# Optimization experiments

Measured on AMD Instinct MI355X. Metric: run time of the kernel, lower is better.

## Reference

```python
import jax, jax.numpy as jnp
import numpy as np
from jax import lax

KERNEL_SIZE = 3
DILATION = 1
STRIDE = 1


def setup_inputs() -> dict:
    key = jax.random.key(0)
    k1, k2, k3, k4 = jax.random.split(key, 4)
    B, C_in, L = 8, 256, 4096
    C_out = 256
    out_len = L - DILATION * (KERNEL_SIZE - 1)  # 4094, 'valid' conv
    x = jax.random.normal(k1, (B, C_in, L), dtype=jnp.float32)
    offsets = jax.random.normal(k2, (B, 1, out_len, KERNEL_SIZE), dtype=jnp.float32)
    fan_in = C_in * KERNEL_SIZE
    weight = jax.random.normal(k3, (C_out, C_in, KERNEL_SIZE), dtype=jnp.float32) / np.sqrt(fan_in)
    bias = jax.random.normal(k4, (C_out,), dtype=jnp.float32) / np.sqrt(fan_in)
    return {"x": x, "offsets": offsets, "weight": weight, "bias": bias}


def reference(x, offsets, weight, bias):
    # x: [B, C, L]; offsets: [B, 1, out_len, K]; weight: [C_out, C, K]
    B, C, L = x.shape
    out_len = offsets.shape[-2]
    K = weight.shape[-1]
    dtype = x.dtype

    # dilated kernel sample positions: linspace(0, dilation*(K-1), K)
    dil_pos = (jnp.arange(K, dtype=dtype) * DILATION)  # [K]
    t0s = (jnp.arange(out_len, dtype=dtype) * STRIDE)[:, None]  # [out_len, 1]

    # continuous sample locations, constrained to [t0, t0 + max(dil_pos)]
    T = t0s + dil_pos + offsets  # [B, 1, out_len, K]
    T = jnp.clip(T, t0s, t0s + dil_pos[-1])

    # integer neighbors (indices are non-differentiable)
    U0 = lax.stop_gradient(
        jnp.clip(jnp.floor(T), 0, L - 2).astype(jnp.int32)
    )  # [B, 1, out_len, K]
    U1 = U0 + 1

    def gather(idx):
        # idx: [B, 1, out_len, K] -> gather along L, broadcast over channels
        flat = jnp.broadcast_to(idx.reshape(B, 1, out_len * K), (B, C, out_len * K))
        return jnp.take_along_axis(x, flat, axis=2).reshape(B, C, out_len, K)

    x0 = gather(U0)
    x1 = gather(U1)

    # linear-interpolation weights (tent kernel), broadcast [B,1,out_len,K]
    w0 = jnp.maximum(0.0, 1.0 - jnp.abs(U0.astype(dtype) - T))
    w1 = jnp.maximum(0.0, 1.0 - jnp.abs(U1.astype(dtype) - T))

    interp = w0 * x0 + w1 * x1  # [B, C, out_len, K]

    # conv1d(flatten(interp), weight, stride=K) == per-position K-tap contraction
    out = jnp.einsum("bctk,ock->bot", interp, weight) + bias[None, :, None]
    return out  # [B, C_out, out_len]
```

## Files before the change

kernel.cpp:

```cpp
#include <hip/hip_runtime.h>
#include <stdint.h>


constexpr int CIN  = 256;
constexpr int LX   = 4096;
constexpr int KT   = 3;
constexpr int OUTL = 4094;
constexpr int COUT = 256;
constexpr int WPOS = 68;
constexpr int NQ   = 24;
constexpr int EPIW = 68;
constexpr int NIT  = 2176;

typedef __attribute__((ext_vector_type(8))) short bf16x8;
typedef __attribute__((ext_vector_type(4))) float f32x4;
typedef __attribute__((ext_vector_type(16))) float f32x16;

__device__ __forceinline__ short f2bf(float f) {
  union { float f; uint32_t u; } v; v.f = f;
  return (short)((v.u + 0x8000u) >> 16);
}
__device__ __forceinline__ float4 loadx4(const float* p, int l) {
  if (l + 3 < LX) return *(const float4*)(p + l);
  float4 v; v.x = v.y = v.z = v.w = 0.f;
  if (l + 0 < LX) v.x = p[l + 0];
  if (l + 1 < LX) v.y = p[l + 1];
  if (l + 2 < LX) v.z = p[l + 2];
  return v;
}

__global__ __launch_bounds__(256) void pack_weights_kernel(
    const float* __restrict__ w, short* __restrict__ ap) {
  const int gid = blockIdx.x * 256 + threadIdx.x;
  if (gid >= NQ * 2 * 8 * 64) return;
  const int l   = gid & 63;
  const int mf  = (gid >> 6) & 7;
  const int h   = (gid >> 9) & 1;
  const int q   = gid >> 10;
  const int ch  = q / 12;
  const int ks  = q % 12;
  const int tap = ks >> 2;
  const int c0  = ch * 128 + (ks & 3) * 32 + h * 16 + (l >> 5) * 8;
  const int row = mf * 32 + (l & 31);
  bf16x8 v;
  #pragma unroll
  for (int j = 0; j < 8; ++j) {
    v[j] = f2bf(w[((size_t)row * CIN + c0 + j) * KT + tap]);
  }
  *(bf16x8*)(ap + (size_t)gid * 8) = v;
}

__global__ __launch_bounds__(512, 4) void deform_gemm_kernel(
    const float* __restrict__ x, const float* __restrict__ off,
    const short* __restrict__ ap, const float* __restrict__ bias,
    float* __restrict__ out) {

  __shared__ __align__(16) char smem[34816 + 16384 + 1024];
  float* Xs    = (float*)smem;
  short* Bp    = (short*)(smem + 34816);
  float* Epi   = (float*)smem;
  float* biasS = (float*)(smem + 51200);

  const int tid  = threadIdx.x;
  const int lane = tid & 63;
  const int wid  = tid >> 6;
  const int l31  = lane & 31;
  const int lh   = lane >> 5;

  const int b    = blockIdx.x & 7;
  const int rest = blockIdx.x >> 3;
  const int th   = rest & 1;
  const int tt   = rest >> 1;
  const int t0   = tt * 128 + th * 64;

  float w0m[3], w1m[3];
  int   d0m[3];
  {
    const int t = t0 + (tid & 63);
    #pragma unroll
    for (int k = 0; k < KT; ++k) {
      float w0 = 0.f, w1 = 0.f; int d0 = 0;
      if (t < OUTL) {
        const float o = off[((size_t)b * OUTL + t) * KT + k];
        float T = (float)(t + k) + o;
        T = fminf(fmaxf(T, (float)t), (float)(t + 2));
        int U0 = (int)T;
        if (U0 > LX - 2) U0 = LX - 2;
        w1 = T - (float)U0;
        w0 = 1.f - w1;
        d0 = U0 - t0;
      }
      w0m[k] = w0; w1m[k] = w1; d0m[k] = d0;
    }
  }
  if (tid < COUT) biasS[tid] = bias[tid];

  f32x16 acc0 = {0.f,0.f,0.f,0.f,0.f,0.f,0.f,0.f,0.f,0.f,0.f,0.f,0.f,0.f,0.f,0.f};
  f32x16 acc1 = {0.f,0.f,0.f,0.f,0.f,0.f,0.f,0.f,0.f,0.f,0.f,0.f,0.f,0.f,0.f,0.f};

  const float* xb = x + (size_t)b * CIN * LX;

  const short* apw = ap + wid * 512 + lane * 8;
  bf16x8 aC0 = *(const bf16x8*)apw;
  bf16x8 aC1 = *(const bf16x8*)(apw + 4096);

  #pragma unroll 1
  for (int ch = 0; ch < 2; ++ch) {
    if (ch) __syncthreads();
    #pragma unroll
    for (int r = 0; r < 5; ++r) {
      const int idx = r * 512 + tid;
      if (idx < NIT) {
        const int c = idx / 17, g = idx - c * 17;
        const float4 v = loadx4(xb + (size_t)(ch * 128 + c) * LX, t0 + 4 * g);
        *(float4*)&Xs[c * WPOS + 4 * g] = v;
      }
    }
    __syncthreads();

    #pragma unroll
    for (int tap = 0; tap < KT; ++tap) {
      if (tap) __syncthreads();

      {
        const int tq = tid & 63;
        const int cb = (tid >> 6) * 16;
        const float w0 = w0m[tap], w1 = w1m[tap];
        const int   d0 = d0m[tap];
        const int swt = (tq & 7) << 3;
        bf16x8 o1, o2;
        #pragma unroll
        for (int j = 0; j < 8; ++j) {
          const float xa0 = Xs[(cb + j) * WPOS + d0];
          const float xa1 = Xs[(cb + j) * WPOS + d0 + 1];
          o1[j] = f2bf(xa0 * w0 + xa1 * w1);
        }
        *(bf16x8*)&Bp[(tq * 128 + cb) ^ swt] = o1;
        #pragma unroll
        for (int j = 0; j < 8; ++j) {
          const float xb0 = Xs[(cb + 8 + j) * WPOS + d0];
          const float xb1 = Xs[(cb + 8 + j) * WPOS + d0 + 1];
          o2[j] = f2bf(xb0 * w0 + xb1 * w1);
        }
        *(bf16x8*)&Bp[(tq * 128 + cb + 8) ^ swt] = o2;
      }
      __syncthreads();

      #pragma unroll 1
      for (int csub = 0; csub < 4; ++csub) {
        const int q  = ch * 12 + tap * 4 + csub;
        const int qn = q < NQ - 1 ? q + 1 : NQ - 1;
        const bf16x8 aN0 = *(const bf16x8*)(apw + (size_t)qn * 8192);
        const bf16x8 aN1 = *(const bf16x8*)(apw + (size_t)qn * 8192 + 4096);

        const int cbase = csub * 32 + lh * 8;
        const int ta = l31,      swa = (ta & 7) << 3;
        const int tb = 32 + l31, swb = (tb & 7) << 3;
        {
          const bf16x8 b00 = *(const bf16x8*)&Bp[(ta * 128 + cbase) ^ swa];
          const bf16x8 b10 = *(const bf16x8*)&Bp[(tb * 128 + cbase) ^ swb];
          acc0 = __builtin_amdgcn_mfma_f32_32x32x16_bf16(aC0, b00, acc0, 0, 0, 0);
          acc1 = __builtin_amdgcn_mfma_f32_32x32x16_bf16(aC0, b10, acc1, 0, 0, 0);
        }
        {
          const bf16x8 b01 = *(const bf16x8*)&Bp[(ta * 128 + cbase + 16) ^ swa];
          const bf16x8 b11 = *(const bf16x8*)&Bp[(tb * 128 + cbase + 16) ^ swb];
          acc0 = __builtin_amdgcn_mfma_f32_32x32x16_bf16(aC1, b01, acc0, 0, 0, 0);
          acc1 = __builtin_amdgcn_mfma_f32_32x32x16_bf16(aC1, b11, acc1, 0, 0, 0);
        }
        aC0 = aN0; aC1 = aN1;
      }
    }
  }

  const size_t obase = (size_t)b * COUT * OUTL;
  #pragma unroll
  for (int p = 0; p < 4; ++p) {
    __syncthreads();
    if ((wid >> 1) == p) {
      const int lrb = (wid & 1) * 32;
      #pragma unroll
      for (int r = 0; r < 16; ++r) {
        const int rowl = (r & 3) + 8 * (r >> 2) + 4 * lh;
        const int grow = p * 64 + lrb + rowl;
        Epi[(lrb + rowl) * EPIW + l31]      = acc0[r] + biasS[grow];
        Epi[(lrb + rowl) * EPIW + 32 + l31] = acc1[r] + biasS[grow];
      }
    }
    __syncthreads();
    const int rr = tid >> 3;
    const int c8 = (tid & 7) * 8;
    float* op = out + obase + (size_t)(p * 64 + rr) * OUTL + t0 + c8;
    const f32x4 v0 = *(const f32x4*)&Epi[rr * EPIW + c8];
    const f32x4 v1 = *(const f32x4*)&Epi[rr * EPIW + c8 + 4];
    if (t0 + c8 + 7 < OUTL) {
      *(f32x4*)op = v0;
      *(f32x4*)(op + 4) = v1;
    } else {
      #pragma unroll
      for (int e = 0; e < 4; ++e) {
        if (t0 + c8 + e < OUTL)     op[e]     = v0[e];
        if (t0 + c8 + 4 + e < OUTL) op[4 + e] = v1[e];
      }
    }
  }
}

extern "C" void kernel_launch(void* const* d_in, const int* in_sizes, int n_in,
                              void* d_out, int out_size, void* d_ws, size_t ws_size,
                              hipStream_t stream) {
  const float* x    = (const float*)d_in[0];
  const float* off  = (const float*)d_in[1];
  const float* wgt  = (const float*)d_in[2];
  const float* bias = (const float*)d_in[3];
  float* out  = (float*)d_out;
  short* ap   = (short*)d_ws;

  pack_weights_kernel<<<dim3(NQ * 2 * 8 * 64 / 256), dim3(256), 0, stream>>>(wgt, ap);
  deform_gemm_kernel<<<dim3(512), dim3(512), 0, stream>>>(x, off, ap, bias, out);
}
```

Baseline: 40.39 us.

## Stage X as transposed bf16 and double-buffer interpolated B tiles

The staged input tile is now stored as bf16 in a position-major, XOR-swizzled layout, so the interpolation step reads two 8-wide vectors instead of sixteen scalar fp32 LDS loads. The interpolated B operand is double-buffered: the next tap's tile is built while MFMAs consume the current one, and the second channel half's input is staged during the last tap's MFMAs. This is meant to hide LDS build and global load latency behind matrix work and cut barriers. The cost is an extra bf16 rounding of x before interpolation, which slightly changes numerics.

```diff
diff --git a/kernel.cpp b/kernel.cpp
--- a/kernel.cpp
+++ b/kernel.cpp
@@ -7,10 +7,10 @@
 constexpr int KT   = 3;
 constexpr int OUTL = 4094;
 constexpr int COUT = 256;
-constexpr int WPOS = 68;
 constexpr int NQ   = 24;
 constexpr int EPIW = 68;
 constexpr int NIT  = 2176;
+constexpr int BPH  = 8192;
 
 typedef __attribute__((ext_vector_type(8))) short bf16x8;
 typedef __attribute__((ext_vector_type(4))) float f32x4;
@@ -19,6 +19,11 @@
 __device__ __forceinline__ short f2bf(float f) {
   union { float f; uint32_t u; } v; v.f = f;
   return (short)((v.u + 0x8000u) >> 16);
+}
+__device__ __forceinline__ float bf2f(short s) {
+  union { uint32_t u; float f; } v;
+  v.u = ((uint32_t)(uint16_t)s) << 16;
+  return v.f;
 }
 __device__ __forceinline__ float4 loadx4(const float* p, int l) {
   if (l + 3 < LX) return *(const float4*)(p + l);
@@ -55,11 +60,11 @@
     const short* __restrict__ ap, const float* __restrict__ bias,
     float* __restrict__ out) {
 
-  __shared__ __align__(16) char smem[34816 + 16384 + 1024];
-  float* Xs    = (float*)smem;
-  short* Bp    = (short*)(smem + 34816);
+  __shared__ __align__(16) char smem[17408 + 2 * 16384 + 1024];
+  short* Xt    = (short*)smem;
+  short* BpB   = (short*)(smem + 17408);
   float* Epi   = (float*)smem;
-  float* biasS = (float*)(smem + 51200);
+  float* biasS = (float*)(smem + 50176);
 
   const int tid  = threadIdx.x;
   const int lane = tid & 63;
@@ -104,79 +109,140 @@
   bf16x8 aC0 = *(const bf16x8*)apw;
   bf16x8 aC1 = *(const bf16x8*)(apw + 4096);
 
+  auto stage = [&](int ch) {
+    #pragma unroll
+    for (int pr = 0; pr < 2; ++pr) {
+      const int i0 = pr * 1024 + tid;
+      const int i1 = i0 + 512;
+      const int c0i = i0 / 17, g0 = i0 - c0i * 17;
+      const int c1i = i1 / 17, g1 = i1 - c1i * 17;
+      const float4 v0 = loadx4(xb + (size_t)(ch * 128 + c0i) * LX, t0 + 4 * g0);
+      const float4 v1 = loadx4(xb + (size_t)(ch * 128 + c1i) * LX, t0 + 4 * g1);
+      const float f0e[4] = {v0.x, v0.y, v0.z, v0.w};
+      const float f1e[4] = {v1.x, v1.y, v1.z, v1.w};
+      #pragma unroll
+      for (int e = 0; e < 4; ++e) {
+        const int p0 = g0 * 4 + e;
+        Xt[(p0 * 128 + c0i) ^ ((p0 & 7) << 3)] = f2bf(f0e[e]);
+      }
+      #pragma unroll
+      for (int e = 0; e < 4; ++e) {
+        const int p1 = g1 * 4 + e;
+        Xt[(p1 * 128 + c1i) ^ ((p1 & 7) << 3)] = f2bf(f1e[e]);
+      }
+    }
+    {
+      const int i4 = 2048 + tid;
+      if (i4 < NIT) {
+        const int c = i4 / 17, g = i4 - c * 17;
+        const float4 v = loadx4(xb + (size_t)(ch * 128 + c) * LX, t0 + 4 * g);
+        const float fe[4] = {v.x, v.y, v.z, v.w};
+        #pragma unroll
+        for (int e = 0; e < 4; ++e) {
+          const int pos = g * 4 + e;
+          Xt[(pos * 128 + c) ^ ((pos & 7) << 3)] = f2bf(fe[e]);
+        }
+      }
+    }
+  };
+
+  auto build = [&](short* Bq, int tap) {
+    const int tq = tid & 63;
+    const int cb = (tid >> 6) * 16;
+    const float w0 = w0m[tap], w1 = w1m[tap];
+    const int   d0 = d0m[tap];
+    const int sw0 = (d0 & 7) << 3;
+    const int sw1 = ((d0 + 1) & 7) << 3;
+    const int r0i = d0 * 128, r1i = (d0 + 1) * 128;
+    const int swt = (tq & 7) << 3;
+    {
+      const bf16x8 r0a = *(const bf16x8*)&Xt[(r0i + cb) ^ sw0];
+      const bf16x8 r1a = *(const bf16x8*)&Xt[(r1i + cb) ^ sw1];
+      bf16x8 o1;
+      #pragma unroll
+      for (int j = 0; j < 8; ++j)
+        o1[j] = f2bf(bf2f(r0a[j]) * w0 + bf2f(r1a[j]) * w1);
+      *(bf16x8*)&Bq[(tq * 128 + cb) ^ swt] = o1;
+    }
+    {
+      const bf16x8 r0b = *(const bf16x8*)&Xt[(r0i + cb + 8) ^ sw0];
+      const bf16x8 r1b = *(const bf16x8*)&Xt[(r1i + cb + 8) ^ sw1];
+      bf16x8 o2;
+      #pragma unroll
+      for (int j = 0; j < 8; ++j)
+        o2[j] = f2bf(bf2f(r0b[j]) * w0 + bf2f(r1b[j]) * w1);
+      *(bf16x8*)&Bq[(tq * 128 + cb + 8) ^ swt] = o2;
+    }
+  };
+
+  auto ksteps = [&](const short* Bq, int p) {
+    #pragma unroll 1
+    for (int csub = 0; csub < 4; ++csub) {
+      const int q  = p * 4 + csub;
+      const int qn = q < NQ - 1 ? q + 1 : NQ - 1;
+      const bf16x8 aN0 = *(const bf16x8*)(apw + (size_t)qn * 8192);
+      const bf16x8 aN1 = *(const bf16x8*)(apw + (size_t)qn * 8192 + 4096);
+
+      const int cbase = csub * 32 + lh * 8;
+      const int ta = l31,      swa = (ta & 7) << 3;
+      const int tb = 32 + l31, swb = (tb & 7) << 3;
+      {
+        const bf16x8 b00 = *(const bf16x8*)&Bq[(ta * 128 + cbase) ^ swa];
+        const bf16x8 b10 = *(const bf16x8*)&Bq[(tb * 128 + cbase) ^ swb];
+        acc0 = __builtin_amdgcn_mfma_f32_32x32x16_bf16(aC0, b00, acc0, 0, 0, 0);
+        acc1 = __builtin_amdgcn_mfma_f32_32x32x16_bf16(aC0, b10, acc1, 0, 0, 0);
+      }
+      {
+        const bf16x8 b01 = *(const bf16x8*)&Bq[(ta * 128 + cbase + 16) ^ swa];
+        const bf16x8 b11 = *(const bf16x8*)&Bq[(tb * 128 + cbase + 16) ^ swb];
+        acc0 = __builtin_amdgcn_mfma_f32_32x32x16_bf16(aC1, b01, acc0, 0, 0, 0);
+        acc1 = __builtin_amdgcn_mfma_f32_32x32x16_bf16(aC1, b11, acc1, 0, 0, 0);
+      }
+      aC0 = aN0; aC1 = aN1;
+    }
+  };
+
+  stage(0);
+  __syncthreads();
+  build(BpB, 0);
+  __syncthreads();
+
   #pragma unroll 1
   for (int ch = 0; ch < 2; ++ch) {
-    if (ch) __syncthreads();
-    #pragma unroll
-    for (int r = 0; r < 5; ++r) {
-      const int idx = r * 512 + tid;
-      if (idx < NIT) {
-        const int c = idx / 17, g = idx - c * 17;
-        const float4 v = loadx4(xb + (size_t)(ch * 128 + c) * LX, t0 + 4 * g);
-        *(float4*)&Xs[c * WPOS + 4 * g] = v;
-      }
-    }
-    __syncthreads();
-
-    #pragma unroll
-    for (int tap = 0; tap < KT; ++tap) {
-      if (tap) __syncthreads();
-
-      {
-        const int tq = tid & 63;
-        const int cb = (tid >> 6) * 16;
-        const float w0 = w0m[tap], w1 = w1m[tap];
-        const int   d0 = d0m[tap];
-        const int swt = (tq & 7) << 3;
-        bf16x8 o1, o2;
-        #pragma unroll
-        for (int j = 0; j < 8; ++j) {
-          const float xa0 = Xs[(cb + j) * WPOS + d0];
-          const float xa1 = Xs[(cb + j) * WPOS + d0 + 1];
-          o1[j] = f2bf(xa0 * w0 + xa1 * w1);
-        }
-        *(bf16x8*)&Bp[(tq * 128 + cb) ^ swt] = o1;
-        #pragma unroll
-        for (int j = 0; j < 8; ++j) {
-          const float xb0 = Xs[(cb + 8 + j) * WPOS + d0];
-          const float xb1 = Xs[(cb + 8 + j) * WPOS + d0 + 1];
-          o2[j] = f2bf(xb0 * w0 + xb1 * w1);
-        }
-        *(bf16x8*)&Bp[(tq * 128 + cb + 8) ^ swt] = o2;
-      }
+    {
+      const int p = ch * 3;
+      short* cur = BpB + (p & 1) * BPH;
+      short* nxt = BpB + ((p + 1) & 1) * BPH;
+      if (ch == 1) {
+        build(cur, 0);
+        __syncthreads();
+      }
+      build(nxt, 1);
+      ksteps(cur, p);
       __syncthreads();
-
-      #pragma unroll 1
-      for (int csub = 0; csub < 4; ++csub) {
-        const int q  = ch * 12 + tap * 4 + csub;
-        const int qn = q < NQ - 1 ? q + 1 : NQ - 1;
-        const bf16x8 aN0 = *(const bf16x8*)(apw + (size_t)qn * 8192);
-        const bf16x8 aN1 = *(const bf16x8*)(apw + (size_t)qn * 8192 + 4096);
-
-        const int cbase = csub * 32 + lh * 8;
-        const int ta = l31,      swa = (ta & 7) << 3;
-        const int tb = 32 + l31, swb = (tb & 7) << 3;
-        {
-          const bf16x8 b00 = *(const bf16x8*)&Bp[(ta * 128 + cbase) ^ swa];
-          const bf16x8 b10 = *(const bf16x8*)&Bp[(tb * 128 + cbase) ^ swb];
-          acc0 = __builtin_amdgcn_mfma_f32_32x32x16_bf16(aC0, b00, acc0, 0, 0, 0);
-          acc1 = __builtin_amdgcn_mfma_f32_32x32x16_bf16(aC0, b10, acc1, 0, 0, 0);
-        }
-        {
-          const bf16x8 b01 = *(const bf16x8*)&Bp[(ta * 128 + cbase + 16) ^ swa];
-          const bf16x8 b11 = *(const bf16x8*)&Bp[(tb * 128 + cbase + 16) ^ swb];
-          acc0 = __builtin_amdgcn_mfma_f32_32x32x16_bf16(aC1, b01, acc0, 0, 0, 0);
-          acc1 = __builtin_amdgcn_mfma_f32_32x32x16_bf16(aC1, b11, acc1, 0, 0, 0);
-        }
-        aC0 = aN0; aC1 = aN1;
-      }
+    }
+    {
+      const int p = ch * 3 + 1;
+      short* cur = BpB + (p & 1) * BPH;
+      short* nxt = BpB + ((p + 1) & 1) * BPH;
+      if (ch == 0) build(nxt, 2);
+      else         build(nxt, 2);
+      ksteps(cur, p);
+      __syncthreads();
+    }
+    {
+      const int p = ch * 3 + 2;
+      short* cur = BpB + (p & 1) * BPH;
+      if (ch == 0) stage(1);
+      ksteps(cur, p);
+      __syncthreads();
     }
   }
 
   const size_t obase = (size_t)b * COUT * OUTL;
   #pragma unroll
   for (int p = 0; p < 4; ++p) {
-    __syncthreads();
+    if (p) __syncthreads();
     if ((wid >> 1) == p) {
       const int lrb = (wid & 1) * 32;
       #pragma unroll
```

Result: slower. 42.37 us (+4.9%).

## Fuse interpolation into MFMA operand loads with bf16 transposed x tile

Applied to the files above, without the earlier changes.

Stores the x tile in shared memory as swizzled bf16 in position-major layout. Each wave now builds its own interpolated A operand in registers directly before the MFMA, which removes the separate interpolated-B staging buffer and the per-tap barriers. The operand roles are swapped: interpolated activations become the A matrix and weights are read from global as the B matrix, with the epilogue transposed to match. Shared memory use shrinks and the launch bounds change, at the cost of double rounding of x to bf16, repeated interpolation work per wave, and unprefetched global weight loads inside the loop.

```diff
diff --git a/kernel.cpp b/kernel.cpp
--- a/kernel.cpp
+++ b/kernel.cpp
@@ -7,9 +7,8 @@
 constexpr int KT   = 3;
 constexpr int OUTL = 4094;
 constexpr int COUT = 256;
-constexpr int WPOS = 68;
 constexpr int NQ   = 24;
-constexpr int EPIW = 68;
+constexpr int EPIT = 65;
 constexpr int NIT  = 2176;
 
 typedef __attribute__((ext_vector_type(8))) short bf16x8;
@@ -19,6 +18,11 @@
 __device__ __forceinline__ short f2bf(float f) {
   union { float f; uint32_t u; } v; v.f = f;
   return (short)((v.u + 0x8000u) >> 16);
+}
+__device__ __forceinline__ float bf2f(short s) {
+  union { uint32_t u; float f; } v;
+  v.u = ((uint32_t)(uint16_t)s) << 16;
+  return v.f;
 }
 __device__ __forceinline__ float4 loadx4(const float* p, int l) {
   if (l + 3 < LX) return *(const float4*)(p + l);
@@ -50,16 +54,15 @@
   *(bf16x8*)(ap + (size_t)gid * 8) = v;
 }
 
-__global__ __launch_bounds__(512, 4) void deform_gemm_kernel(
+__global__ __launch_bounds__(512, 2) void deform_gemm_kernel(
     const float* __restrict__ x, const float* __restrict__ off,
     const short* __restrict__ ap, const float* __restrict__ bias,
     float* __restrict__ out) {
 
-  __shared__ __align__(16) char smem[34816 + 16384 + 1024];
-  float* Xs    = (float*)smem;
-  short* Bp    = (short*)(smem + 34816);
+  __shared__ __align__(16) char smem[17408 + 1024];
+  short* Xt    = (short*)smem;
   float* Epi   = (float*)smem;
-  float* biasS = (float*)(smem + 51200);
+  float* biasS = (float*)(smem + 17408);
 
   const int tid  = threadIdx.x;
   const int lane = tid & 63;
@@ -67,6 +70,9 @@
   const int l31  = lane & 31;
   const int lh   = lane >> 5;
 
+  const int tfrag = wid & 1;
+  const int og    = wid >> 1;
+
   const int b    = blockIdx.x & 7;
   const int rest = blockIdx.x >> 3;
   const int th   = rest & 1;
@@ -76,7 +82,7 @@
   float w0m[3], w1m[3];
   int   d0m[3];
   {
-    const int t = t0 + (tid & 63);
+    const int t = t0 + tfrag * 32 + l31;
     #pragma unroll
     for (int k = 0; k < KT; ++k) {
       float w0 = 0.f, w1 = 0.f; int d0 = 0;
@@ -100,75 +106,69 @@
 
   const float* xb = x + (size_t)b * CIN * LX;
 
-  const short* apw = ap + wid * 512 + lane * 8;
-  bf16x8 aC0 = *(const bf16x8*)apw;
-  bf16x8 aC1 = *(const bf16x8*)(apw + 4096);
-
   #pragma unroll 1
   for (int ch = 0; ch < 2; ++ch) {
     if (ch) __syncthreads();
     #pragma unroll
     for (int r = 0; r < 5; ++r) {
       const int idx = r * 512 + tid;
-      if (idx < NIT) {
+      if (r < 4 || idx < NIT) {
         const int c = idx / 17, g = idx - c * 17;
         const float4 v = loadx4(xb + (size_t)(ch * 128 + c) * LX, t0 + 4 * g);
-        *(float4*)&Xs[c * WPOS + 4 * g] = v;
+        const float fe[4] = {v.x, v.y, v.z, v.w};
+        #pragma unroll
+        for (int e = 0; e < 4; ++e) {
+          const int pos = g * 4 + e;
+          Xt[(pos * 128 + c) ^ ((pos & 7) << 3)] = f2bf(fe[e]);
+        }
       }
     }
     __syncthreads();
 
     #pragma unroll
     for (int tap = 0; tap < KT; ++tap) {
-      if (tap) __syncthreads();
-
-      {
-        const int tq = tid & 63;
-        const int cb = (tid >> 6) * 16;
-        const float w0 = w0m[tap], w1 = w1m[tap];
-        const int   d0 = d0m[tap];
-        const int swt = (tq & 7) << 3;
-        bf16x8 o1, o2;
-        #pragma unroll
-        for (int j = 0; j < 8; ++j) {
-          const float xa0 = Xs[(cb + j) * WPOS + d0];
-          const float xa1 = Xs[(cb + j) * WPOS + d0 + 1];
-          o1[j] = f2bf(xa0 * w0 + xa1 * w1);
-        }
-        *(bf16x8*)&Bp[(tq * 128 + cb) ^ swt] = o1;
-        #pragma unroll
-        for (int j = 0; j < 8; ++j) {
-          const float xb0 = Xs[(cb + 8 + j) * WPOS + d0];
-          const float xb1 = Xs[(cb + 8 + j) * WPOS + d0 + 1];
-          o2[j] = f2bf(xb0 * w0 + xb1 * w1);
-        }
-        *(bf16x8*)&Bp[(tq * 128 + cb + 8) ^ swt] = o2;
-      }
-      __syncthreads();
+      const float w0 = w0m[tap];
+      const float w1 = w1m[tap];
+      const int   d0 = d0m[tap];
+      const int sw0 = (d0 & 7) << 3;
+      const int sw1 = ((d0 + 1) & 7) << 3;
+      const int r0i = d0 * 128, r1i = (d0 + 1) * 128;
 
       #pragma unroll 1
       for (int csub = 0; csub < 4; ++csub) {
-        const int q  = ch * 12 + tap * 4 + csub;
-        const int qn = q < NQ - 1 ? q + 1 : NQ - 1;
-        const bf16x8 aN0 = *(const bf16x8*)(apw + (size_t)qn * 8192);
-        const bf16x8 aN1 = *(const bf16x8*)(apw + (size_t)qn * 8192 + 4096);
-
-        const int cbase = csub * 32 + lh * 8;
-        const int ta = l31,      swa = (ta & 7) << 3;
-        const int tb = 32 + l31, swb = (tb & 7) << 3;
-        {
-          const bf16x8 b00 = *(const bf16x8*)&Bp[(ta * 128 + cbase) ^ swa];
-          const bf16x8 b10 = *(const bf16x8*)&Bp[(tb * 128 + cbase) ^ swb];
-          acc0 = __builtin_amdgcn_mfma_f32_32x32x16_bf16(aC0, b00, acc0, 0, 0, 0);
-          acc1 = __builtin_amdgcn_mfma_f32_32x32x16_bf16(aC0, b10, acc1, 0, 0, 0);
-        }
-        {
-          const bf16x8 b01 = *(const bf16x8*)&Bp[(ta * 128 + cbase + 16) ^ swa];
-          const bf16x8 b11 = *(const bf16x8*)&Bp[(tb * 128 + cbase + 16) ^ swb];
-          acc0 = __builtin_amdgcn_mfma_f32_32x32x16_bf16(aC1, b01, acc0, 0, 0, 0);
-          acc1 = __builtin_amdgcn_mfma_f32_32x32x16_bf16(aC1, b11, acc1, 0, 0, 0);
-        }
-        aC0 = aN0; aC1 = aN1;
+        const int q = ch * 12 + tap * 4 + csub;
+
+        bf16x8 aA0, aA1;
+        {
+          const int cs = csub * 32 + lh * 8;
+          const bf16x8 r0 = *(const bf16x8*)&Xt[(r0i + cs) ^ sw0];
+          const bf16x8 r1 = *(const bf16x8*)&Xt[(r1i + cs) ^ sw1];
+          #pragma unroll
+          for (int j = 0; j < 8; ++j)
+            aA0[j] = f2bf(bf2f(r0[j]) * w0 + bf2f(r1[j]) * w1);
+        }
+        {
+          const int cs = csub * 32 + 16 + lh * 8;
+          const bf16x8 r0 = *(const bf16x8*)&Xt[(r0i + cs) ^ sw0];
+          const bf16x8 r1 = *(const bf16x8*)&Xt[(r1i + cs) ^ sw1];
+          #pragma unroll
+          for (int j = 0; j < 8; ++j)
+            aA1[j] = f2bf(bf2f(r0[j]) * w0 + bf2f(r1[j]) * w1);
+        }
+
+        const short* wq = ap + (size_t)q * 8192 + lane * 8;
+        {
+          const bf16x8 w00 = *(const bf16x8*)(wq + (og * 2) * 512);
+          const bf16x8 w01 = *(const bf16x8*)(wq + 4096 + (og * 2) * 512);
+          acc0 = __builtin_amdgcn_mfma_f32_32x32x16_bf16(aA0, w00, acc0, 0, 0, 0);
+          acc0 = __builtin_amdgcn_mfma_f32_32x32x16_bf16(aA1, w01, acc0, 0, 0, 0);
+        }
+        {
+          const bf16x8 w10 = *(const bf16x8*)(wq + (og * 2 + 1) * 512);
+          const bf16x8 w11 = *(const bf16x8*)(wq + 4096 + (og * 2 + 1) * 512);
+          acc1 = __builtin_amdgcn_mfma_f32_32x32x16_bf16(aA0, w10, acc1, 0, 0, 0);
+          acc1 = __builtin_amdgcn_mfma_f32_32x32x16_bf16(aA1, w11, acc1, 0, 0, 0);
+        }
       }
     }
   }
@@ -177,22 +177,29 @@
   #pragma unroll
   for (int p = 0; p < 4; ++p) {
     __syncthreads();
-    if ((wid >> 1) == p) {
-      const int lrb = (wid & 1) * 32;
+    if (og == p) {
       #pragma unroll
       for (int r = 0; r < 16; ++r) {
-        const int rowl = (r & 3) + 8 * (r >> 2) + 4 * lh;
-        const int grow = p * 64 + lrb + rowl;
-        Epi[(lrb + rowl) * EPIW + l31]      = acc0[r] + biasS[grow];
-        Epi[(lrb + rowl) * EPIW + 32 + l31] = acc1[r] + biasS[grow];
+        const int trow = (r & 3) + 8 * (r >> 2) + 4 * lh;
+        const int tl   = tfrag * 32 + trow;
+        Epi[tl * EPIT + l31] = acc0[r] + biasS[p * 64 + l31];
+      }
+      #pragma unroll
+      for (int r = 0; r < 16; ++r) {
+        const int trow = (r & 3) + 8 * (r >> 2) + 4 * lh;
+        const int tl   = tfrag * 32 + trow;
+        Epi[tl * EPIT + 32 + l31] = acc1[r] + biasS[p * 64 + 32 + l31];
       }
     }
     __syncthreads();
     const int rr = tid >> 3;
     const int c8 = (tid & 7) * 8;
+    float vals[8];
+    #pragma unroll
+    for (int m = 0; m < 8; ++m) vals[m] = Epi[(c8 + m) * EPIT + rr];
+    const f32x4 v0 = {vals[0], vals[1], vals[2], vals[3]};
+    const f32x4 v1 = {vals[4], vals[5], vals[6], vals[7]};
     float* op = out + obase + (size_t)(p * 64 + rr) * OUTL + t0 + c8;
-    const f32x4 v0 = *(const f32x4*)&Epi[rr * EPIW + c8];
-    const f32x4 v1 = *(const f32x4*)&Epi[rr * EPIW + c8 + 4];
     if (t0 + c8 + 7 < OUTL) {
       *(f32x4*)op = v0;
       *(f32x4*)(op + 4) = v1;
```

After: 52.26 us. 1.29x slower.

## Stage full-channel x tile as transposed bf16 in LDS and vectorize interpolation

Applied to the files above, without the earlier changes.

Loads all 256 input channels of the x tile at once, converts to bf16 and stores it position-major with an XOR swizzle. This lets the interpolation step read 8 channels per vector LDS load instead of scalar strided float reads. It also removes the two-pass channel loop and halves the per-tap barriers. The cost is a larger LDS footprint and a lower occupancy bound (3 blocks instead of 4). Rounding x to bf16 before interpolating adds a second rounding step, which slightly lowers accuracy.

```diff
diff --git a/kernel.cpp b/kernel.cpp
--- a/kernel.cpp
+++ b/kernel.cpp
@@ -7,10 +7,10 @@
 constexpr int KT   = 3;
 constexpr int OUTL = 4094;
 constexpr int COUT = 256;
-constexpr int WPOS = 68;
 constexpr int NQ   = 24;
 constexpr int EPIW = 68;
-constexpr int NIT  = 2176;
+constexpr int CW   = 256;
+constexpr int NST  = 4352;
 
 typedef __attribute__((ext_vector_type(8))) short bf16x8;
 typedef __attribute__((ext_vector_type(4))) float f32x4;
@@ -19,6 +19,11 @@
 __device__ __forceinline__ short f2bf(float f) {
   union { float f; uint32_t u; } v; v.f = f;
   return (short)((v.u + 0x8000u) >> 16);
+}
+__device__ __forceinline__ float bf2f(short s) {
+  union { uint32_t u; float f; } v;
+  v.u = ((uint32_t)(uint16_t)s) << 16;
+  return v.f;
 }
 __device__ __forceinline__ float4 loadx4(const float* p, int l) {
   if (l + 3 < LX) return *(const float4*)(p + l);
@@ -50,16 +55,16 @@
   *(bf16x8*)(ap + (size_t)gid * 8) = v;
 }
 
-__global__ __launch_bounds__(512, 4) void deform_gemm_kernel(
+__global__ __launch_bounds__(512, 3) void deform_gemm_kernel(
     const float* __restrict__ x, const float* __restrict__ off,
     const short* __restrict__ ap, const float* __restrict__ bias,
     float* __restrict__ out) {
 
-  __shared__ __align__(16) char smem[34816 + 16384 + 1024];
-  float* Xs    = (float*)smem;
+  __shared__ __align__(16) char smem[34816 + 32768 + 1024];
+  short* Xt    = (short*)smem;
   short* Bp    = (short*)(smem + 34816);
   float* Epi   = (float*)smem;
-  float* biasS = (float*)(smem + 51200);
+  float* biasS = (float*)(smem + 67584);
 
   const int tid  = threadIdx.x;
   const int lane = tid & 63;
@@ -104,72 +109,84 @@
   bf16x8 aC0 = *(const bf16x8*)apw;
   bf16x8 aC1 = *(const bf16x8*)(apw + 4096);
 
-  #pragma unroll 1
-  for (int ch = 0; ch < 2; ++ch) {
-    if (ch) __syncthreads();
+  #pragma unroll
+  for (int rb = 0; rb < 3; ++rb) {
+    float4 xv[3]; int cc[3], gg[3];
     #pragma unroll
-    for (int r = 0; r < 5; ++r) {
-      const int idx = r * 512 + tid;
-      if (idx < NIT) {
-        const int c = idx / 17, g = idx - c * 17;
-        const float4 v = loadx4(xb + (size_t)(ch * 128 + c) * LX, t0 + 4 * g);
-        *(float4*)&Xs[c * WPOS + 4 * g] = v;
+    for (int j = 0; j < 3; ++j) {
+      const int idx = (rb * 3 + j) * 512 + tid;
+      if (idx < NST) {
+        cc[j] = idx / 17; gg[j] = idx - cc[j] * 17;
+        xv[j] = loadx4(xb + (size_t)cc[j] * LX, t0 + 4 * gg[j]);
+      }
+    }
+    #pragma unroll
+    for (int j = 0; j < 3; ++j) {
+      const int idx = (rb * 3 + j) * 512 + tid;
+      if (idx < NST) {
+        const float fe[4] = {xv[j].x, xv[j].y, xv[j].z, xv[j].w};
+        #pragma unroll
+        for (int e = 0; e < 4; ++e) {
+          const int pos = gg[j] * 4 + e;
+          Xt[(pos * CW + cc[j]) ^ ((pos & 15) << 3)] = f2bf(fe[e]);
+        }
+      }
+    }
+  }
+  __syncthreads();
+
+  #pragma unroll
+  for (int tap = 0; tap < KT; ++tap) {
+    if (tap) __syncthreads();
+
+    {
+      const int tq  = tid & 63;
+      const int cb0 = wid * 32;
+      const float w0 = w0m[tap], w1 = w1m[tap];
+      const int   d0 = d0m[tap];
+      const int r0i = d0 * CW, r1i = (d0 + 1) * CW;
+      const int s0  = (d0 & 15) << 3;
+      const int s1  = ((d0 + 1) & 15) << 3;
+      const int st  = (tq & 15) << 3;
+      #pragma unroll
+      for (int g = 0; g < 4; ++g) {
+        const int cb = cb0 + g * 8;
+        const bf16x8 ra = *(const bf16x8*)&Xt[(r0i + cb) ^ s0];
+        const bf16x8 rb = *(const bf16x8*)&Xt[(r1i + cb) ^ s1];
+        bf16x8 o;
+        #pragma unroll
+        for (int j = 0; j < 8; ++j)
+          o[j] = f2bf(bf2f(ra[j]) * w0 + bf2f(rb[j]) * w1);
+        *(bf16x8*)&Bp[(tq * CW + cb) ^ st] = o;
       }
     }
     __syncthreads();
 
-    #pragma unroll
-    for (int tap = 0; tap < KT; ++tap) {
-      if (tap) __syncthreads();
-
+    #pragma unroll 1
+    for (int kc = 0; kc < 8; ++kc) {
+      const int q  = tap * 4 + (kc >> 2) * 12 + (kc & 3);
+      const int kn = kc + 1;
+      const int qn = (kc < 7) ? (tap * 4 + (kn >> 2) * 12 + (kn & 3))
+                              : (tap < 2 ? (tap + 1) * 4 : q);
+      const bf16x8 aN0 = *(const bf16x8*)(apw + (size_t)qn * 8192);
+      const bf16x8 aN1 = *(const bf16x8*)(apw + (size_t)qn * 8192 + 4096);
+
+      const int cg = (kc >> 2) * 128 + (kc & 3) * 32 + lh * 8;
+      const int ta = l31,      swa = (ta & 15) << 3;
+      const int tb = 32 + l31, swb = (tb & 15) << 3;
       {
-        const int tq = tid & 63;
-        const int cb = (tid >> 6) * 16;
-        const float w0 = w0m[tap], w1 = w1m[tap];
-        const int   d0 = d0m[tap];
-        const int swt = (tq & 7) << 3;
-        bf16x8 o1, o2;
-        #pragma unroll
-        for (int j = 0; j < 8; ++j) {
-          const float xa0 = Xs[(cb + j) * WPOS + d0];
-          const float xa1 = Xs[(cb + j) * WPOS + d0 + 1];
-          o1[j] = f2bf(xa0 * w0 + xa1 * w1);
-        }
-        *(bf16x8*)&Bp[(tq * 128 + cb) ^ swt] = o1;
-        #pragma unroll
-        for (int j = 0; j < 8; ++j) {
-          const float xb0 = Xs[(cb + 8 + j) * WPOS + d0];
-          const float xb1 = Xs[(cb + 8 + j) * WPOS + d0 + 1];
-          o2[j] = f2bf(xb0 * w0 + xb1 * w1);
-        }
-        *(bf16x8*)&Bp[(tq * 128 + cb + 8) ^ swt] = o2;
-      }
-      __syncthreads();
-
-      #pragma unroll 1
-      for (int csub = 0; csub < 4; ++csub) {
-        const int q  = ch * 12 + tap * 4 + csub;
-        const int qn = q < NQ - 1 ? q + 1 : NQ - 1;
-        const bf16x8 aN0 = *(const bf16x8*)(apw + (size_t)qn * 8192);
-        const bf16x8 aN1 = *(const bf16x8*)(apw + (size_t)qn * 8192 + 4096);
-
-        const int cbase = csub * 32 + lh * 8;
-        const int ta = l31,      swa = (ta & 7) << 3;
-        const int tb = 32 + l31, swb = (tb & 7) << 3;
-        {
-          const bf16x8 b00 = *(const bf16x8*)&Bp[(ta * 128 + cbase) ^ swa];
-          const bf16x8 b10 = *(const bf16x8*)&Bp[(tb * 128 + cbase) ^ swb];
-          acc0 = __builtin_amdgcn_mfma_f32_32x32x16_bf16(aC0, b00, acc0, 0, 0, 0);
-          acc1 = __builtin_amdgcn_mfma_f32_32x32x16_bf16(aC0, b10, acc1, 0, 0, 0);
-        }
-        {
-          const bf16x8 b01 = *(const bf16x8*)&Bp[(ta * 128 + cbase + 16) ^ swa];
-          const bf16x8 b11 = *(const bf16x8*)&Bp[(tb * 128 + cbase + 16) ^ swb];
-          acc0 = __builtin_amdgcn_mfma_f32_32x32x16_bf16(aC1, b01, acc0, 0, 0, 0);
-          acc1 = __builtin_amdgcn_mfma_f32_32x32x16_bf16(aC1, b11, acc1, 0, 0, 0);
-        }
-        aC0 = aN0; aC1 = aN1;
-      }
+        const bf16x8 b00 = *(const bf16x8*)&Bp[(ta * CW + cg) ^ swa];
+        const bf16x8 b10 = *(const bf16x8*)&Bp[(tb * CW + cg) ^ swb];
+        acc0 = __builtin_amdgcn_mfma_f32_32x32x16_bf16(aC0, b00, acc0, 0, 0, 0);
+        acc1 = __builtin_amdgcn_mfma_f32_32x32x16_bf16(aC0, b10, acc1, 0, 0, 0);
+      }
+      {
+        const bf16x8 b01 = *(const bf16x8*)&Bp[(ta * CW + cg + 16) ^ swa];
+        const bf16x8 b11 = *(const bf16x8*)&Bp[(tb * CW + cg + 16) ^ swb];
+        acc0 = __builtin_amdgcn_mfma_f32_32x32x16_bf16(aC1, b01, acc0, 0, 0, 0);
+        acc1 = __builtin_amdgcn_mfma_f32_32x32x16_bf16(aC1, b11, acc1, 0, 0, 0);
+      }
+      aC0 = aN0; aC1 = aN1;
     }
   }
 
```

New measurement: 41.87 us. +3.7%, slower.
